# Kernel optimization log

Hardware: AMD Instinct MI355X
Metric: run time of the kernel (lower is better)

## Reference

```python
import jax, jax.numpy as jnp
import numpy as np
import math

D_MODEL = 1024
H = 16
D_HEAD = 64  # d_Q = d_K = d_V
B = 2
S = 2048


def setup_inputs() -> dict:
    key = jax.random.key(0)
    ks = jax.random.split(key, 11)
    scale = 1.0 / math.sqrt(D_MODEL)
    q = jax.random.normal(ks[0], (B, S, D_MODEL), dtype=jnp.float32)
    k = jax.random.normal(ks[1], (B, S, D_MODEL), dtype=jnp.float32)
    v = jax.random.normal(ks[2], (B, S, D_MODEL), dtype=jnp.float32)
    mask = jnp.ones((S, S), dtype=jnp.int32)
    # per-head projection weights stacked over the head axis
    Wq = jax.random.normal(ks[3], (H, D_MODEL, D_HEAD), dtype=jnp.float32) * scale
    bq = jax.random.normal(ks[4], (H, D_HEAD), dtype=jnp.float32) * 0.02
    Wk = jax.random.normal(ks[5], (H, D_MODEL, D_HEAD), dtype=jnp.float32) * scale
    bk = jax.random.normal(ks[6], (H, D_HEAD), dtype=jnp.float32) * 0.02
    Wv = jax.random.normal(ks[7], (H, D_MODEL, D_HEAD), dtype=jnp.float32) * scale
    bv = jax.random.normal(ks[8], (H, D_HEAD), dtype=jnp.float32) * 0.02
    Wo = jax.random.normal(ks[9], (H * D_HEAD, D_MODEL), dtype=jnp.float32) * (1.0 / math.sqrt(H * D_HEAD))
    return {"q": q, "k": k, "v": v, "mask": mask,
            "Wq": Wq, "bq": bq, "Wk": Wk, "bk": bk, "Wv": Wv, "bv": bv, "Wo": Wo}


def reference(q, k, v, mask, Wq, bq, Wk, bk, Wv, bv, Wo):
    d_k = Wq.shape[-1]
    # batched per-head projections: [B,S,D] x [H,D,E] -> [B,H,S,E]
    Qh = jnp.einsum('bsd,hde->bhse', q, Wq) + bq[None, :, None, :]
    Kh = jnp.einsum('bsd,hde->bhse', k, Wk) + bk[None, :, None, :]
    Vh = jnp.einsum('bsd,hde->bhse', v, Wv) + bv[None, :, None, :]
    scores = jnp.einsum('bhse,bhte->bhst', Qh, Kh) / jnp.sqrt(jnp.float32(d_k))
    scores = jnp.where(mask == 0, jnp.float32(-1e9), scores)
    attn = jax.nn.softmax(scores, axis=-1)
    ctx = jnp.einsum('bhst,bhte->bhse', attn, Vh)
    # concat heads along feature dim: [B,S,H*E]
    ctx = ctx.transpose(0, 2, 1, 3).reshape(q.shape[0], q.shape[1], -1)
    return ctx @ Wo
```

## Files before the change

### kernel.cpp

```cpp
#include <hip/hip_runtime.h>
#include <math.h>

#define S_LEN 2048
#define DM    1024
#define NH    16
#define DH    64
#define BATCH 2
#define MROWS 4096
#define LOG2E 1.44269504088896340736f

typedef __attribute__((ext_vector_type(8))) short short8;
typedef __attribute__((ext_vector_type(4))) float f32x4;

__device__ __forceinline__ unsigned short f2bf(float f) {
    unsigned int u = __float_as_uint(f);
    u += 0x7FFFu + ((u >> 16) & 1u);
    return (unsigned short)(u >> 16);
}

__device__ __forceinline__ void gload16(const void* g, void* lds) {
    __builtin_amdgcn_global_load_lds((const __attribute__((address_space(1))) void*)g,
                                     (__attribute__((address_space(3))) void*)lds,
                                     16, 0, 0);
}

__global__ void initflag_kernel(int* flag) {
    if (threadIdx.x == 0 && blockIdx.x == 0) *flag = 1;
}

__global__ __launch_bounds__(256) void convert3(
    const float* __restrict__ q, const float* __restrict__ k, const float* __restrict__ v,
    unsigned short* __restrict__ qb, unsigned short* __restrict__ kb, unsigned short* __restrict__ vb,
    int n4)
{
    int i = blockIdx.x * 256 + threadIdx.x;
    if (i >= n4) return;
    float4 a = ((const float4*)q)[i];
    float4 b = ((const float4*)k)[i];
    float4 c = ((const float4*)v)[i];
    ((ushort4*)qb)[i] = make_ushort4(f2bf(a.x), f2bf(a.y), f2bf(a.z), f2bf(a.w));
    ((ushort4*)kb)[i] = make_ushort4(f2bf(b.x), f2bf(b.y), f2bf(b.z), f2bf(b.w));
    ((ushort4*)vb)[i] = make_ushort4(f2bf(c.x), f2bf(c.y), f2bf(c.z), f2bf(c.w));
}

__global__ __launch_bounds__(256) void transpose_bf16(
    const float* __restrict__ in, unsigned short* __restrict__ out, int R, int C)
{
    __shared__ float tile[32][33];
    const size_t slab = (size_t)blockIdx.z * R * C;
    const int r0 = blockIdx.x * 32;
    const int c0 = blockIdx.y * 32;
    const int tr = threadIdx.x >> 5;
    const int tc = threadIdx.x & 31;
#pragma unroll
    for (int j = 0; j < 32; j += 8)
        tile[tr + j][tc] = in[slab + (size_t)(r0 + tr + j) * C + c0 + tc];
    __syncthreads();
#pragma unroll
    for (int j = 0; j < 32; j += 8)
        out[slab + (size_t)(c0 + tr + j) * R + r0 + tc] = f2bf(tile[tc][tr + j]);
}

__global__ __launch_bounds__(256) void maskbits_kernel(
    const int* __restrict__ mask, unsigned int* __restrict__ bits, int* __restrict__ flag)
{
    int widx = blockIdx.x * 256 + threadIdx.x;
    const int4* src = (const int4*)(mask + (size_t)widx * 32);
    unsigned int wb = 0;
#pragma unroll
    for (int j = 0; j < 8; ++j) {
        int4 vv = src[j];
        wb |= (vv.x != 0 ? 1u : 0u) << (4 * j);
        wb |= (vv.y != 0 ? 1u : 0u) << (4 * j + 1);
        wb |= (vv.z != 0 ? 1u : 0u) << (4 * j + 2);
        wb |= (vv.w != 0 ? 1u : 0u) << (4 * j + 3);
    }
    bits[widx] = wb;
    if (wb != 0xFFFFFFFFu) atomicAnd(flag, 0);
}

template<int MODE>
__global__ __launch_bounds__(256) void gemm128(
    const unsigned short* __restrict__ Aall,
    const unsigned short* __restrict__ Btall,
    const float* __restrict__ bias0, const float* __restrict__ bias1, const float* __restrict__ bias2,
    void* __restrict__ outp)
{
    __shared__ __attribute__((aligned(16))) unsigned short Asm[128 * 64];
    __shared__ __attribute__((aligned(16))) unsigned short Bsm[128 * 64];
    char* AsmC = (char*)Asm;
    char* BsmC = (char*)Bsm;
    const int tid  = threadIdx.x;
    const int w    = tid >> 6;
    const int lane = tid & 63;
    const int m0 = blockIdx.y * 128;
    const int n0 = blockIdx.x * 128;
    const int z  = blockIdx.z;

    const char* Ac = (const char*)(Aall + (size_t)z * MROWS * DM);
    const char* Bc = (const char*)(Btall + (size_t)z * DM * DM);

    int arow[4], akof[4];
#pragma unroll
    for (int r = 0; r < 4; ++r) {
        int L = r * 4096 + tid * 16;
        int a = L ^ (((L >> 7) & 7) << 4);
        arow[r] = a >> 7;
        akof[r] = a & 127;
    }

    const int wr = (w >> 1) * 64;
    const int wc = (w & 1) * 64;
    int aaddr[4], baddr[4];
#pragma unroll
    for (int f = 0; f < 4; ++f) {
        int rr = wr + f * 16 + (lane & 15);
        aaddr[f] = (rr * 128 + ((lane >> 4) << 4)) ^ ((rr & 7) << 4);
        int rn = wc + f * 16 + (lane & 15);
        baddr[f] = (rn * 128 + ((lane >> 4) << 4)) ^ ((rn & 7) << 4);
    }

    f32x4 acc[4][4] = {};

    for (int kt = 0; kt < 16; ++kt) {
        __syncthreads();
#pragma unroll
        for (int r = 0; r < 4; ++r) {
            gload16(Ac + (size_t)(m0 + arow[r]) * (DM * 2) + kt * 128 + akof[r],
                    AsmC + r * 4096 + w * 1024);
            gload16(Bc + (size_t)(n0 + arow[r]) * (DM * 2) + kt * 128 + akof[r],
                    BsmC + r * 4096 + w * 1024);
        }
        __syncthreads();
#pragma unroll
        for (int ks = 0; ks < 2; ++ks) {
            short8 af[4], bf[4];
#pragma unroll
            for (int f = 0; f < 4; ++f) af[f] = *(const short8*)(AsmC + (aaddr[f] ^ (ks << 6)));
#pragma unroll
            for (int f = 0; f < 4; ++f) bf[f] = *(const short8*)(BsmC + (baddr[f] ^ (ks << 6)));
#pragma unroll
            for (int mf = 0; mf < 4; ++mf)
#pragma unroll
                for (int nf = 0; nf < 4; ++nf)
                    acc[mf][nf] = __builtin_amdgcn_mfma_f32_16x16x32_bf16(af[mf], bf[nf], acc[mf][nf], 0, 0, 0);
        }
    }

    if constexpr (MODE == 0) {
        const float* bias = (z == 0) ? bias0 : (z == 1) ? bias1 : bias2;
        unsigned short* out = ((unsigned short*)outp) + (size_t)z * MROWS * DM;
        float bv[4];
#pragma unroll
        for (int nf = 0; nf < 4; ++nf) bv[nf] = bias[n0 + wc + nf * 16 + (lane & 15)];
#pragma unroll
        for (int mf = 0; mf < 4; ++mf)
#pragma unroll
            for (int nf = 0; nf < 4; ++nf)
#pragma unroll
                for (int i = 0; i < 4; ++i) {
                    int grow = m0 + wr + mf * 16 + ((lane >> 4) << 2) + i;
                    int gcol = n0 + wc + nf * 16 + (lane & 15);
                    float val = acc[mf][nf][i] + bv[nf];
                    int b = grow >> 11, srow = grow & 2047, h = gcol >> 6, e = gcol & 63;
                    out[((size_t)(b * NH + h) * S_LEN + srow) * DH + e] = f2bf(val);
                }
    } else {
        float* out = (float*)outp;
#pragma unroll
        for (int mf = 0; mf < 4; ++mf)
#pragma unroll
            for (int nf = 0; nf < 4; ++nf)
#pragma unroll
                for (int i = 0; i < 4; ++i) {
                    int grow = m0 + wr + mf * 16 + ((lane >> 4) << 2) + i;
                    int gcol = n0 + wc + nf * 16 + (lane & 15);
                    out[(size_t)grow * DM + gcol] = acc[mf][nf][i];
                }
    }
}

__global__ __launch_bounds__(256, 4) void attn_kernel(
    const unsigned short* __restrict__ Qh, const unsigned short* __restrict__ Kh,
    const unsigned short* __restrict__ Vh, unsigned short* __restrict__ ctx,
    const unsigned int* __restrict__ mbits, const int* __restrict__ flag)
{
    __shared__ __attribute__((aligned(16))) char smem[16384 + 16384 + 8192];
    char* KsmB = smem;
    char* VsmB = smem + 16384;
    char* QP   = smem + 32768;

    const int tid  = threadIdx.x;
    const int w    = tid >> 6;
    const int lane = tid & 63;
    const int q0 = blockIdx.x * 64;
    const int bh = blockIdx.y;

    const char* Qb = (const char*)(Qh + (size_t)bh * S_LEN * DH);
    const char* Kb = (const char*)(Kh + (size_t)bh * S_LEN * DH);
    const char* Vb = (const char*)(Vh + (size_t)bh * S_LEN * DH);

#pragma unroll
    for (int r = 0; r < 2; ++r) {
        int L = r * 4096 + tid * 16;
        int a = L ^ (((L >> 7) & 7) << 4);
        gload16(Qb + (size_t)(q0 + (a >> 7)) * 128 + (a & 127), QP + r * 4096 + w * 1024);
    }
    __syncthreads();
    short8 qf[2];
#pragma unroll
    for (int ks = 0; ks < 2; ++ks) {
        int row = w * 16 + (lane & 15);
        int a = row * 128 + ks * 64 + ((lane >> 4) << 4);
        qf[ks] = *(const short8*)(QP + (a ^ ((row & 7) << 4)));
    }
    __syncthreads();

    const bool allones = (*flag) != 0;

    float mstate[4], lstate[4];
#pragma unroll
    for (int i = 0; i < 4; ++i) { mstate[i] = -INFINITY; lstate[i] = 0.f; }
    f32x4 o[4] = {};

    char* Pw = QP + w * 2048;

    const int vp = tid >> 4;
    const int vd0 = (tid & 15) * 4;
    uint2 va[2], vb2[2];

#pragma unroll
    for (int r = 0; r < 2; ++r) {
        int L = r * 4096 + tid * 16;
        int a = L ^ (((L >> 7) & 7) << 4);
        gload16(Kb + (size_t)(a >> 7) * 128 + (a & 127), KsmB + r * 4096 + w * 1024);
    }
#pragma unroll
    for (int r = 0; r < 2; ++r) {
        int t0 = (r * 16 + vp) * 2;
        va[r]  = *(const uint2*)(Vb + (size_t)t0 * 128 + vd0 * 2);
        vb2[r] = *(const uint2*)(Vb + (size_t)(t0 + 1) * 128 + vd0 * 2);
    }
#pragma unroll
    for (int r = 0; r < 2; ++r) {
        int pp = r * 16 + vp;
        int d = vd0;
        int vm0 = (d ^ (d >> 3)) & 7;       int vm1 = ((d+1) ^ ((d+1) >> 3)) & 7;
        int vm2 = ((d+2) ^ ((d+2) >> 3)) & 7; int vm3 = ((d+3) ^ ((d+3) >> 3)) & 7;
        *(unsigned int*)(VsmB + (d+0) * 128 + ((pp * 4) ^ (vm0 << 4))) = (va[r].x & 0xffffu) | (vb2[r].x << 16);
        *(unsigned int*)(VsmB + (d+1) * 128 + ((pp * 4) ^ (vm1 << 4))) = (va[r].x >> 16)     | (vb2[r].x & 0xffff0000u);
        *(unsigned int*)(VsmB + (d+2) * 128 + ((pp * 4) ^ (vm2 << 4))) = (va[r].y & 0xffffu) | (vb2[r].y << 16);
        *(unsigned int*)(VsmB + (d+3) * 128 + ((pp * 4) ^ (vm3 << 4))) = (va[r].y >> 16)     | (vb2[r].y & 0xffff0000u);
    }
    __syncthreads();

    for (int kv = 0; kv < 32; ++kv) {
        char* Kc = KsmB + (kv & 1) * 8192;
        char* Vc = VsmB + (kv & 1) * 8192;
        char* Kn = KsmB + ((kv & 1) ^ 1) * 8192;
        char* Vn = VsmB + ((kv & 1) ^ 1) * 8192;
        const bool more = (kv + 1 < 32);
        const int kv0 = kv * 64;

        if (more) {
            const int kv1 = kv0 + 64;
#pragma unroll
            for (int r = 0; r < 2; ++r) {
                int L = r * 4096 + tid * 16;
                int a = L ^ (((L >> 7) & 7) << 4);
                gload16(Kb + (size_t)(kv1 + (a >> 7)) * 128 + (a & 127), Kn + r * 4096 + w * 1024);
            }
#pragma unroll
            for (int r = 0; r < 2; ++r) {
                int t0 = kv1 + (r * 16 + vp) * 2;
                va[r]  = *(const uint2*)(Vb + (size_t)t0 * 128 + vd0 * 2);
                vb2[r] = *(const uint2*)(Vb + (size_t)(t0 + 1) * 128 + vd0 * 2);
            }
        }

        f32x4 sc[4] = {};
#pragma unroll
        for (int ks = 0; ks < 2; ++ks) {
            short8 kf[4];
#pragma unroll
            for (int nf = 0; nf < 4; ++nf) {
                int trow = nf * 16 + (lane & 15);
                int a = trow * 128 + ks * 64 + ((lane >> 4) << 4);
                kf[nf] = *(const short8*)(Kc + (a ^ ((trow & 7) << 4)));
            }
#pragma unroll
            for (int nf = 0; nf < 4; ++nf)
                sc[nf] = __builtin_amdgcn_mfma_f32_16x16x32_bf16(qf[ks], kf[nf], sc[nf], 0, 0, 0);
        }

#pragma unroll
        for (int nf = 0; nf < 4; ++nf)
#pragma unroll
            for (int i = 0; i < 4; ++i) sc[nf][i] *= 0.125f;
        if (!allones) {
#pragma unroll
            for (int i = 0; i < 4; ++i) {
                int row = q0 + w * 16 + ((lane >> 4) << 2) + i;
#pragma unroll
                for (int nf = 0; nf < 4; ++nf) {
                    int t = kv0 + nf * 16 + (lane & 15);
                    if (!((mbits[row * (S_LEN / 32) + (t >> 5)] >> (t & 31)) & 1u))
                        sc[nf][i] = -1e9f;
                }
            }
        }

#pragma unroll
        for (int i = 0; i < 4; ++i) {
            float pm = fmaxf(fmaxf(sc[0][i], sc[1][i]), fmaxf(sc[2][i], sc[3][i]));
            pm = fmaxf(pm, __shfl_xor(pm, 1));
            pm = fmaxf(pm, __shfl_xor(pm, 2));
            pm = fmaxf(pm, __shfl_xor(pm, 4));
            pm = fmaxf(pm, __shfl_xor(pm, 8));
            float mnew = fmaxf(mstate[i], pm);
            float corr = exp2f((mstate[i] - mnew) * LOG2E);
            float rs = 0.f;
#pragma unroll
            for (int nf = 0; nf < 4; ++nf) {
                float p = exp2f((sc[nf][i] - mnew) * LOG2E);
                sc[nf][i] = p;
                rs += p;
            }
            rs += __shfl_xor(rs, 1);
            rs += __shfl_xor(rs, 2);
            rs += __shfl_xor(rs, 4);
            rs += __shfl_xor(rs, 8);
            lstate[i] = lstate[i] * corr + rs;
            mstate[i] = mnew;
#pragma unroll
            for (int nfo = 0; nfo < 4; ++nfo) o[nfo][i] *= corr;
        }

#pragma unroll
        for (int nf = 0; nf < 4; ++nf)
#pragma unroll
            for (int i = 0; i < 4; ++i) {
                int prow = ((lane >> 4) << 2) + i;
                int a = prow * 128 + (nf * 16 + (lane & 15)) * 2;
                *(unsigned short*)(Pw + (a ^ (((prow ^ (prow >> 2)) & 7) << 4))) = f2bf(sc[nf][i]);
            }

#pragma unroll
        for (int ks = 0; ks < 2; ++ks) {
            int prow = lane & 15;
            int ap = prow * 128 + ks * 64 + ((lane >> 4) << 4);
            short8 pa = *(const short8*)(Pw + (ap ^ (((prow ^ (prow >> 2)) & 7) << 4)));
#pragma unroll
            for (int nfo = 0; nfo < 4; ++nfo) {
                int d = nfo * 16 + (lane & 15);
                int vm = (d ^ (d >> 3)) & 7;
                int p0 = ks * 16 + ((lane >> 4) << 2);
                short8 vf = *(const short8*)(Vc + d * 128 + ((p0 * 4) ^ (vm << 4)));
                o[nfo] = __builtin_amdgcn_mfma_f32_16x16x32_bf16(pa, vf, o[nfo], 0, 0, 0);
            }
        }

        if (more) {
#pragma unroll
            for (int r = 0; r < 2; ++r) {
                int pp = r * 16 + vp;
                int d = vd0;
                int vm0 = (d ^ (d >> 3)) & 7;       int vm1 = ((d+1) ^ ((d+1) >> 3)) & 7;
                int vm2 = ((d+2) ^ ((d+2) >> 3)) & 7; int vm3 = ((d+3) ^ ((d+3) >> 3)) & 7;
                *(unsigned int*)(Vn + (d+0) * 128 + ((pp * 4) ^ (vm0 << 4))) = (va[r].x & 0xffffu) | (vb2[r].x << 16);
                *(unsigned int*)(Vn + (d+1) * 128 + ((pp * 4) ^ (vm1 << 4))) = (va[r].x >> 16)     | (vb2[r].x & 0xffff0000u);
                *(unsigned int*)(Vn + (d+2) * 128 + ((pp * 4) ^ (vm2 << 4))) = (va[r].y & 0xffffu) | (vb2[r].y << 16);
                *(unsigned int*)(Vn + (d+3) * 128 + ((pp * 4) ^ (vm3 << 4))) = (va[r].y >> 16)     | (vb2[r].y & 0xffff0000u);
            }
        }
        __syncthreads();
    }

    const int b = bh >> 4;
    const int h = bh & 15;
#pragma unroll
    for (int nfo = 0; nfo < 4; ++nfo)
#pragma unroll
        for (int i = 0; i < 4; ++i) {
            int srow = q0 + w * 16 + ((lane >> 4) << 2) + i;
            int e = nfo * 16 + (lane & 15);
            float val = o[nfo][i] / lstate[i];
            ctx[((size_t)(b * S_LEN + srow)) * DM + h * DH + e] = f2bf(val);
        }
}

extern "C" void kernel_launch(void* const* d_in, const int* in_sizes, int n_in,
                              void* d_out, int out_size, void* d_ws, size_t ws_size,
                              hipStream_t stream)
{
    const float* q    = (const float*)d_in[0];
    const float* k    = (const float*)d_in[1];
    const float* v    = (const float*)d_in[2];
    const int*   mask = (const int*)d_in[3];
    const float* Wq   = (const float*)d_in[4];
    const float* bq   = (const float*)d_in[5];
    const float* Wk   = (const float*)d_in[6];
    const float* bk   = (const float*)d_in[7];
    const float* Wv   = (const float*)d_in[8];
    const float* bv   = (const float*)d_in[9];
    const float* Wo   = (const float*)d_in[10];

    char* W = (char*)d_ws;
    unsigned short* qkvb = (unsigned short*)(W + 0);
    unsigned short* ctx  = (unsigned short*)(W + 0);
    unsigned short* Wt   = (unsigned short*)(W + 25165824);
    unsigned short* QKVh = (unsigned short*)(W + 31457280);
    unsigned short* Wot  = (unsigned short*)(W + 56623104);
    unsigned int*   mbits= (unsigned int*)(W + 58720256);
    int*            flag = (int*)(W + 59244544);
    if (ws_size < (size_t)59244548) return;

    initflag_kernel<<<1, 64, 0, stream>>>(flag);
    convert3<<<4096, 256, 0, stream>>>(q, k, v, qkvb, qkvb + 4194304, qkvb + 8388608, 1048576);
    transpose_bf16<<<dim3(32, 2, 16), 256, 0, stream>>>(Wq, Wt,            1024, 64);
    transpose_bf16<<<dim3(32, 2, 16), 256, 0, stream>>>(Wk, Wt + 1048576,  1024, 64);
    transpose_bf16<<<dim3(32, 2, 16), 256, 0, stream>>>(Wv, Wt + 2097152,  1024, 64);
    transpose_bf16<<<dim3(32, 32, 1), 256, 0, stream>>>(Wo, Wot,           1024, 1024);
    maskbits_kernel<<<512, 256, 0, stream>>>(mask, mbits, flag);
    gemm128<0><<<dim3(8, 32, 3), 256, 0, stream>>>(qkvb, Wt, bq, bk, bv, (void*)QKVh);
    attn_kernel<<<dim3(32, 32), 256, 0, stream>>>(QKVh, QKVh + 4194304, QKVh + 8388608, ctx, mbits, flag);
    gemm128<1><<<dim3(8, 32, 1), 256, 0, stream>>>(ctx, Wot, nullptr, nullptr, nullptr, d_out);
}
```

Before: 349.9 us.

## Transpose QK^T MFMA layout, fold softmax scale into Q, lazy max rescaling

Folds the 1/sqrt(d) scale into the Q projection epilogue so the per-tile score scaling goes away. Swaps the MFMA operands so each lane holds one query row, which turns the row max/sum reductions into mostly in-register work with only two cross-lane shuffles, and allows packed 8-byte stores of P to LDS. It also adds a lazy rescale: the running max and the O rescaling are updated only when some lane's new max exceeds the old by more than 8. This trades exactness of the running max for fewer exp and multiply operations, relying on the bounded growth staying within fp32 range.

```diff
diff --git a/kernel.cpp b/kernel.cpp
--- a/kernel.cpp
+++ b/kernel.cpp
@@ -149,6 +149,7 @@
 
     if constexpr (MODE == 0) {
         const float* bias = (z == 0) ? bias0 : (z == 1) ? bias1 : bias2;
+        const float scl = (z == 0) ? 0.125f : 1.0f;
         unsigned short* out = ((unsigned short*)outp) + (size_t)z * MROWS * DM;
         float bv[4];
 #pragma unroll
@@ -161,7 +162,7 @@
                 for (int i = 0; i < 4; ++i) {
                     int grow = m0 + wr + mf * 16 + ((lane >> 4) << 2) + i;
                     int gcol = n0 + wc + nf * 16 + (lane & 15);
-                    float val = acc[mf][nf][i] + bv[nf];
+                    float val = (acc[mf][nf][i] + bv[nf]) * scl;
                     int b = grow >> 11, srow = grow & 2047, h = gcol >> 6, e = gcol & 63;
                     out[((size_t)(b * NH + h) * S_LEN + srow) * DH + e] = f2bf(val);
                 }
@@ -218,9 +219,7 @@
 
     const bool allones = (*flag) != 0;
 
-    float mstate[4], lstate[4];
-#pragma unroll
-    for (int i = 0; i < 4; ++i) { mstate[i] = -INFINITY; lstate[i] = 0.f; }
+    float mstate = -INFINITY, lstate = 0.f;
     f32x4 o[4] = {};
 
     char* Pw = QP + w * 2048;
@@ -290,60 +289,65 @@
             }
 #pragma unroll
             for (int nf = 0; nf < 4; ++nf)
-                sc[nf] = __builtin_amdgcn_mfma_f32_16x16x32_bf16(qf[ks], kf[nf], sc[nf], 0, 0, 0);
-        }
-
-#pragma unroll
-        for (int nf = 0; nf < 4; ++nf)
-#pragma unroll
-            for (int i = 0; i < 4; ++i) sc[nf][i] *= 0.125f;
+                sc[nf] = __builtin_amdgcn_mfma_f32_16x16x32_bf16(kf[nf], qf[ks], sc[nf], 0, 0, 0);
+        }
+
         if (!allones) {
-#pragma unroll
-            for (int i = 0; i < 4; ++i) {
-                int row = q0 + w * 16 + ((lane >> 4) << 2) + i;
-#pragma unroll
-                for (int nf = 0; nf < 4; ++nf) {
-                    int t = kv0 + nf * 16 + (lane & 15);
+            int row = q0 + w * 16 + (lane & 15);
+#pragma unroll
+            for (int nf = 0; nf < 4; ++nf)
+#pragma unroll
+                for (int i = 0; i < 4; ++i) {
+                    int t = kv0 + nf * 16 + ((lane >> 4) << 2) + i;
                     if (!((mbits[row * (S_LEN / 32) + (t >> 5)] >> (t & 31)) & 1u))
                         sc[nf][i] = -1e9f;
                 }
-            }
-        }
-
-#pragma unroll
-        for (int i = 0; i < 4; ++i) {
-            float pm = fmaxf(fmaxf(sc[0][i], sc[1][i]), fmaxf(sc[2][i], sc[3][i]));
-            pm = fmaxf(pm, __shfl_xor(pm, 1));
-            pm = fmaxf(pm, __shfl_xor(pm, 2));
-            pm = fmaxf(pm, __shfl_xor(pm, 4));
-            pm = fmaxf(pm, __shfl_xor(pm, 8));
-            float mnew = fmaxf(mstate[i], pm);
-            float corr = exp2f((mstate[i] - mnew) * LOG2E);
-            float rs = 0.f;
-#pragma unroll
-            for (int nf = 0; nf < 4; ++nf) {
-                float p = exp2f((sc[nf][i] - mnew) * LOG2E);
+        }
+
+        float pmax = sc[0][0];
+#pragma unroll
+        for (int nf = 0; nf < 4; ++nf)
+#pragma unroll
+            for (int i = 0; i < 4; ++i) pmax = fmaxf(pmax, sc[nf][i]);
+        pmax = fmaxf(pmax, __shfl_xor(pmax, 16));
+        pmax = fmaxf(pmax, __shfl_xor(pmax, 32));
+        if (__any(pmax - mstate > 8.0f)) {
+            float mnew = fmaxf(mstate, pmax);
+            float corr = exp2f((mstate - mnew) * LOG2E);
+            mstate = mnew;
+            lstate *= corr;
+#pragma unroll
+            for (int i = 0; i < 4; ++i) {
+                float ci = __shfl(corr, ((lane >> 4) << 2) + i);
+#pragma unroll
+                for (int nfo = 0; nfo < 4; ++nfo) o[nfo][i] *= ci;
+            }
+        }
+        float rs = 0.f;
+#pragma unroll
+        for (int nf = 0; nf < 4; ++nf)
+#pragma unroll
+            for (int i = 0; i < 4; ++i) {
+                float p = exp2f((sc[nf][i] - mstate) * LOG2E);
                 sc[nf][i] = p;
                 rs += p;
             }
-            rs += __shfl_xor(rs, 1);
-            rs += __shfl_xor(rs, 2);
-            rs += __shfl_xor(rs, 4);
-            rs += __shfl_xor(rs, 8);
-            lstate[i] = lstate[i] * corr + rs;
-            mstate[i] = mnew;
-#pragma unroll
-            for (int nfo = 0; nfo < 4; ++nfo) o[nfo][i] *= corr;
-        }
-
-#pragma unroll
-        for (int nf = 0; nf < 4; ++nf)
-#pragma unroll
-            for (int i = 0; i < 4; ++i) {
-                int prow = ((lane >> 4) << 2) + i;
-                int a = prow * 128 + (nf * 16 + (lane & 15)) * 2;
-                *(unsigned short*)(Pw + (a ^ (((prow ^ (prow >> 2)) & 7) << 4))) = f2bf(sc[nf][i]);
-            }
+        rs += __shfl_xor(rs, 16);
+        rs += __shfl_xor(rs, 32);
+        lstate += rs;
+
+        {
+            int qr = lane & 15;
+            int swz = ((qr ^ (qr >> 2)) & 7) << 4;
+#pragma unroll
+            for (int nf = 0; nf < 4; ++nf) {
+                unsigned int lo = (unsigned int)f2bf(sc[nf][0]) | ((unsigned int)f2bf(sc[nf][1]) << 16);
+                unsigned int hi = (unsigned int)f2bf(sc[nf][2]) | ((unsigned int)f2bf(sc[nf][3]) << 16);
+                int a = qr * 128 + (nf * 16 + ((lane >> 4) << 2)) * 2;
+                uint2 pv2; pv2.x = lo; pv2.y = hi;
+                *(uint2*)(Pw + (a ^ swz)) = pv2;
+            }
+        }
 
 #pragma unroll
         for (int ks = 0; ks < 2; ++ks) {
@@ -378,13 +382,16 @@
 
     const int b = bh >> 4;
     const int h = bh & 15;
+    float li[4];
+#pragma unroll
+    for (int i = 0; i < 4; ++i) li[i] = __shfl(lstate, ((lane >> 4) << 2) + i);
 #pragma unroll
     for (int nfo = 0; nfo < 4; ++nfo)
 #pragma unroll
         for (int i = 0; i < 4; ++i) {
             int srow = q0 + w * 16 + ((lane >> 4) << 2) + i;
             int e = nfo * 16 + (lane & 15);
-            float val = o[nfo][i] / lstate[i];
+            float val = o[nfo][i] / li[i];
             ctx[((size_t)(b * S_LEN + srow)) * DM + h * DH + e] = f2bf(val);
         }
 }
```

After: 299.6 us. 1.17x faster.
